# Performance work log

Hardware: AMD Instinct MI355X
Metric: run time of the kernel (lower is better)

## Reference

```python
import jax, jax.numpy as jnp
import numpy as np

N_NODES = 50000
N_EDGES = 800000
F_IN = 128
HID = 256
K = 5
N_GRAPHS = 64


def setup_inputs() -> dict:
    key = jax.random.key(0)
    ks = jax.random.split(key, 16)
    x = jax.random.normal(ks[0], (N_NODES, F_IN), dtype=jnp.float32)
    edge_index = jax.random.randint(ks[1], (2, N_EDGES), 0, N_NODES, dtype=jnp.int32)
    edge_weight = jax.random.uniform(ks[2], (N_EDGES,), dtype=jnp.float32)
    batch = jnp.sort(jax.random.randint(ks[3], (N_NODES,), 0, N_GRAPHS, dtype=jnp.int32))
    s = 0.05
    W1 = jax.random.normal(ks[4], (K, F_IN, HID), dtype=jnp.float32) * s
    b1 = jnp.zeros((HID,), dtype=jnp.float32)
    W2 = jax.random.normal(ks[5], (K, HID, HID), dtype=jnp.float32) * s
    b2 = jnp.zeros((HID,), dtype=jnp.float32)
    W3 = jax.random.normal(ks[6], (K, HID, HID), dtype=jnp.float32) * s
    b3 = jnp.zeros((HID,), dtype=jnp.float32)
    lw1 = jax.random.normal(ks[7], (HID, HID), dtype=jnp.float32) * s
    lb1 = jnp.zeros((HID,), dtype=jnp.float32)
    lw2 = jax.random.normal(ks[8], (HID, 1), dtype=jnp.float32) * s
    lb2 = jnp.zeros((1,), dtype=jnp.float32)
    return dict(x=x, edge_index=edge_index, edge_weight=edge_weight, batch=batch,
                W1=W1, b1=b1, W2=W2, b2=b2, W3=W3, b3=b3,
                lw1=lw1, lb1=lb1, lw2=lw2, lb2=lb2)


def _lap_weights(edge_index, edge_weight, num_nodes):
    # PyG ChebConv with normalization='sym', lambda_max=2.0:
    # L_hat = 2*L/lambda_max - I = -D^{-1/2} A D^{-1/2} on the off-diagonal,
    # zero diagonal. Degree via scatter on edge_index[0].
    src, dst = edge_index[0], edge_index[1]
    deg = jax.ops.segment_sum(edge_weight, src, num_segments=num_nodes)
    dis = jnp.where(deg > 0, jax.lax.rsqrt(jnp.maximum(deg, 1e-30)), 0.0)
    return -(dis[src] * edge_weight * dis[dst])


def _cheb_conv(x, src, dst, lap_w, W, b):
    # propagate: gather from src, weight, scatter-add to dst
    n = x.shape[0]
    prop = lambda z: jax.ops.segment_sum(lap_w[:, None] * z[src], dst, num_segments=n)
    Tx0 = x
    out = Tx0 @ W[0]
    Tx1 = prop(x)
    out = out + Tx1 @ W[1]
    for k in range(2, W.shape[0]):
        Tx2 = 2.0 * prop(Tx1) - Tx0
        out = out + Tx2 @ W[k]
        Tx0, Tx1 = Tx1, Tx2
    return out + b


def reference(x, edge_index, edge_weight, batch, W1, b1, W2, b2, W3, b3, lw1, lb1, lw2, lb2):
    src, dst = edge_index[0], edge_index[1]
    lap_w = _lap_weights(edge_index, edge_weight, x.shape[0])
    h = jax.nn.relu(_cheb_conv(x, src, dst, lap_w, W1, b1))
    h = _cheb_conv(h, src, dst, lap_w, W2, b2)
    h = jax.nn.relu(_cheb_conv(h, src, dst, lap_w, W3, b3))
    # global mean pool over graphs in the batch
    sums = jax.ops.segment_sum(h, batch, num_segments=N_GRAPHS)
    cnts = jax.ops.segment_sum(jnp.ones((h.shape[0],), h.dtype), batch, num_segments=N_GRAPHS)
    g = sums / jnp.maximum(cnts, 1.0)[:, None]
    g = jax.nn.relu(g)  # dropout is identity in eval mode
    g = g @ lw1 + lb1
    g = g @ lw2 + lb2
    return jax.nn.sigmoid(g)
```

## Files before the change

### kernel.cpp

```cpp
#include <hip/hip_runtime.h>
#include <math.h>

typedef unsigned int uint;
typedef unsigned short ushort;
typedef __bf16 bf16x8 __attribute__((ext_vector_type(8)));
typedef float f32x4 __attribute__((ext_vector_type(4)));
typedef __attribute__((address_space(1))) const void gvoid;
typedef __attribute__((address_space(3))) void svoid;

__device__ __forceinline__ float b2f(ushort u) {
  uint v = ((uint)u) << 16;
  return __uint_as_float(v);
}
__device__ __forceinline__ ushort f2b(float f) {
  uint u = __float_as_uint(f);
  u += 0x7FFFu + ((u >> 16) & 1u);
  return (ushort)(u >> 16);
}
__device__ __forceinline__ uint pack2(float a, float b) {
  return (uint)f2b(a) | ((uint)f2b(b) << 16);
}


__global__ void edge_kernel(const int* __restrict__ src, const int* __restrict__ dst,
                            const float* __restrict__ w, float* __restrict__ deg,
                            int* __restrict__ cnt, int ne) {
  int e = blockIdx.x * blockDim.x + threadIdx.x;
  if (e < ne) {
    atomicAdd(&deg[src[e]], w[e]);
    atomicAdd(&cnt[dst[e]], 1);
  }
}

__global__ __launch_bounds__(256) void node_kernel(float* __restrict__ deg,
                                                   const int* __restrict__ cnt,
                                                   int* __restrict__ rowstart,
                                                   int* __restrict__ cursor,
                                                   int* __restrict__ total,
                                                   const int* __restrict__ batch,
                                                   int nb, int ng, int* __restrict__ bnd) {
  __shared__ int ls[256];
  __shared__ int base;
  int tid = threadIdx.x;
  int i = blockIdx.x * 256 + tid;
  int c = (i < nb) ? cnt[i] : 0;
  ls[tid] = c;
  __syncthreads();
  for (int off = 1; off < 256; off <<= 1) {
    int v = (tid >= off) ? ls[tid - off] : 0;
    __syncthreads();
    ls[tid] += v;
    __syncthreads();
  }
  if (tid == 255) base = atomicAdd(total, ls[255]);
  __syncthreads();
  if (i < nb) {
    int pos = base + ls[tid] - c;
    rowstart[i] = pos;
    cursor[i] = pos;
    float d = deg[i];
    deg[i] = d > 0.f ? rsqrtf(fmaxf(d, 1e-30f)) : 0.f;
  }
  if (blockIdx.x == 0 && tid <= ng) {
    int lo = 0, hi = nb;
    while (lo < hi) {
      int mid = (lo + hi) >> 1;
      if (batch[mid] < tid) lo = mid + 1; else hi = mid;
    }
    bnd[tid] = lo;
  }
}

__global__ void scatter_kernel(const int* __restrict__ src, const int* __restrict__ dst,
                               const float* __restrict__ w, const float* __restrict__ dis,
                               int* __restrict__ cursor, int2* __restrict__ cv, int ne) {
  int e = blockIdx.x * blockDim.x + threadIdx.x;
  if (e < ne) {
    int d = dst[e], s = src[e];
    int pos = atomicAdd(&cursor[d], 1);
    float v = -(dis[s] * w[e] * dis[d]);
    cv[pos] = make_int2(s, __float_as_int(v));
  }
}


__global__ void xcvt_kernel(const float* __restrict__ x, uint* __restrict__ o, int total) {
  int i = blockIdx.x * blockDim.x + threadIdx.x;
  if (i < total) {
    float2 v = *(const float2*)(x + (size_t)i * 2);
    o[i] = pack2(v.x, v.y);
  }
}

__global__ void wprep_kernel(const float* __restrict__ W, ushort* __restrict__ WT,
                             int shift, int Ktot, int total) {
  int id = blockIdx.x * blockDim.x + threadIdx.x;
  if (id >= total) return;
  int n = id / Ktot;
  int k = id - n * Ktot;
  int fin = k & ((1 << shift) - 1);
  int ord = k >> shift;
  WT[id] = f2b(W[(size_t)(ord << shift) * 256 + (size_t)fin * 256 + n]);
}

__global__ void wprep2_kernel(const float* __restrict__ W2, ushort* __restrict__ WT2,
                              const float* __restrict__ W3, ushort* __restrict__ WT3,
                              int tot) {
  int id = blockIdx.x * blockDim.x + threadIdx.x;
  if (id >= 2 * tot) return;
  const float* W = (id < tot) ? W2 : W3;
  ushort* WT = (id < tot) ? WT2 : WT3;
  int t = (id < tot) ? id : id - tot;
  int n = t / 1280;
  int k = t - n * 1280;
  int fin = k & 255;
  int ord = k >> 8;
  WT[t] = f2b(W[(size_t)(ord << 8) * 256 + (size_t)fin * 256 + n]);
}


template <int WIDE>
__global__ __launch_bounds__(256) void spmm_wave(const int* __restrict__ rowstart,
                                                 const int* __restrict__ rowcnt,
                                                 const int2* __restrict__ cv,
                                                 const uint* __restrict__ X,
                                                 uint* __restrict__ out,
                                                 const uint* __restrict__ sub,
                                                 float alpha, int nb) {
  int row = blockIdx.x * 4 + (threadIdx.x >> 6);
  if (row >= nb) return;
  int lane = threadIdx.x & 63;
  int e0 = __builtin_amdgcn_readfirstlane(rowstart[row]);
  int cnt = __builtin_amdgcn_readfirstlane(rowcnt[row]);
  int e1 = e0 + cnt;
  float a0 = 0.f, a1 = 0.f, a2 = 0.f, a3 = 0.f;
  int e = e0;
  if (WIDE) {
    const uint2* Xr = (const uint2*)X;
    for (; e + 2 <= e1; e += 2) {
      int2 p0 = cv[e], p1 = cv[e + 1];
      int c0 = __builtin_amdgcn_readfirstlane(p0.x);
      float v0 = __uint_as_float(__builtin_amdgcn_readfirstlane((uint)p0.y));
      int c1 = __builtin_amdgcn_readfirstlane(p1.x);
      float v1 = __uint_as_float(__builtin_amdgcn_readfirstlane((uint)p1.y));
      uint2 g0 = Xr[(size_t)c0 * 64 + lane];
      uint2 g1 = Xr[(size_t)c1 * 64 + lane];
      a0 = fmaf(v0, b2f((ushort)(g0.x & 0xFFFF)), a0);
      a1 = fmaf(v0, b2f((ushort)(g0.x >> 16)), a1);
      a2 = fmaf(v0, b2f((ushort)(g0.y & 0xFFFF)), a2);
      a3 = fmaf(v0, b2f((ushort)(g0.y >> 16)), a3);
      a0 = fmaf(v1, b2f((ushort)(g1.x & 0xFFFF)), a0);
      a1 = fmaf(v1, b2f((ushort)(g1.x >> 16)), a1);
      a2 = fmaf(v1, b2f((ushort)(g1.y & 0xFFFF)), a2);
      a3 = fmaf(v1, b2f((ushort)(g1.y >> 16)), a3);
    }
    if (e < e1) {
      int2 p0 = cv[e];
      int c0 = __builtin_amdgcn_readfirstlane(p0.x);
      float v0 = __uint_as_float(__builtin_amdgcn_readfirstlane((uint)p0.y));
      uint2 g0 = Xr[(size_t)c0 * 64 + lane];
      a0 = fmaf(v0, b2f((ushort)(g0.x & 0xFFFF)), a0);
      a1 = fmaf(v0, b2f((ushort)(g0.x >> 16)), a1);
      a2 = fmaf(v0, b2f((ushort)(g0.y & 0xFFFF)), a2);
      a3 = fmaf(v0, b2f((ushort)(g0.y >> 16)), a3);
    }
    float r0 = alpha * a0, r1 = alpha * a1, r2 = alpha * a2, r3 = alpha * a3;
    if (sub) {
      uint2 s = ((const uint2*)sub)[(size_t)row * 64 + lane];
      r0 -= b2f((ushort)(s.x & 0xFFFF));
      r1 -= b2f((ushort)(s.x >> 16));
      r2 -= b2f((ushort)(s.y & 0xFFFF));
      r3 -= b2f((ushort)(s.y >> 16));
    }
    ((uint2*)out)[(size_t)row * 64 + lane] = make_uint2(pack2(r0, r1), pack2(r2, r3));
  } else {
    for (; e + 2 <= e1; e += 2) {
      int2 p0 = cv[e], p1 = cv[e + 1];
      int c0 = __builtin_amdgcn_readfirstlane(p0.x);
      float v0 = __uint_as_float(__builtin_amdgcn_readfirstlane((uint)p0.y));
      int c1 = __builtin_amdgcn_readfirstlane(p1.x);
      float v1 = __uint_as_float(__builtin_amdgcn_readfirstlane((uint)p1.y));
      uint g0 = X[(size_t)c0 * 64 + lane];
      uint g1 = X[(size_t)c1 * 64 + lane];
      a0 = fmaf(v0, b2f((ushort)(g0 & 0xFFFF)), a0);
      a1 = fmaf(v0, b2f((ushort)(g0 >> 16)), a1);
      a0 = fmaf(v1, b2f((ushort)(g1 & 0xFFFF)), a0);
      a1 = fmaf(v1, b2f((ushort)(g1 >> 16)), a1);
    }
    if (e < e1) {
      int2 p0 = cv[e];
      int c0 = __builtin_amdgcn_readfirstlane(p0.x);
      float v0 = __uint_as_float(__builtin_amdgcn_readfirstlane((uint)p0.y));
      uint g0 = X[(size_t)c0 * 64 + lane];
      a0 = fmaf(v0, b2f((ushort)(g0 & 0xFFFF)), a0);
      a1 = fmaf(v0, b2f((ushort)(g0 >> 16)), a1);
    }
    float r0 = alpha * a0, r1 = alpha * a1;
    if (sub) {
      uint s = sub[(size_t)row * 64 + lane];
      r0 -= b2f((ushort)(s & 0xFFFF));
      r1 -= b2f((ushort)(s >> 16));
    }
    out[(size_t)row * 64 + lane] = pack2(r0, r1);
  }
}


struct APtrs { const ushort* p[5]; };

template <int RELU, int SHIFT>
__global__ __launch_bounds__(256, 2) void gemm_mfma(APtrs ap, const ushort* __restrict__ WT,
                                                    const float* __restrict__ bias,
                                                    ushort* __restrict__ C, int M, int Ktot) {
  constexpr int LDA = 1 << SHIFT;
  __shared__ __align__(16) char lAb[16384];
  __shared__ __align__(16) char lBb[16384];
  int tid = threadIdx.x;
  int lane = tid & 63, w = tid >> 6;
  int wr = w >> 1, wc = w & 1;
  int row0 = blockIdx.x * 128, col0 = blockIdx.y * 128;

  f32x4 acc[4][4];
#pragma unroll
  for (int i = 0; i < 4; ++i)
#pragma unroll
    for (int n = 0; n < 4; ++n) acc[i][n] = {0.f, 0.f, 0.f, 0.f};

  for (int k0 = 0; k0 < Ktot; k0 += 64) {
    const ushort* Ab = ap.p[k0 >> SHIFT];
    int ka = k0 & (LDA - 1);
    __syncthreads();
#pragma unroll
    for (int c = 0; c < 4; ++c) {
      int base = c * 4096 + w * 1024;
      int off = base + lane * 16;
      int row = off >> 7, within = off & 127;
      int lw = within ^ ((row & 7) << 4);
      int grow = row0 + row; if (grow >= M) grow = M - 1;
      const ushort* g = Ab + (size_t)grow * LDA + ka + (lw >> 1);
      __builtin_amdgcn_global_load_lds((gvoid*)g, (svoid*)(lAb + base), 16, 0, 0);
    }
#pragma unroll
    for (int c = 0; c < 4; ++c) {
      int base = c * 4096 + w * 1024;
      int off = base + lane * 16;
      int n = off >> 7, within = off & 127;
      int lw = within ^ ((n & 7) << 4);
      const ushort* g = WT + (size_t)(col0 + n) * Ktot + k0 + (lw >> 1);
      __builtin_amdgcn_global_load_lds((gvoid*)g, (svoid*)(lBb + base), 16, 0, 0);
    }
    asm volatile("s_waitcnt vmcnt(0)" ::: "memory");
    __syncthreads();
#pragma unroll
    for (int s = 0; s < 2; ++s) {
      int kb = (s << 6) + ((lane >> 4) << 4);
      bf16x8 af[4], bfr[4];
#pragma unroll
      for (int i = 0; i < 4; ++i) {
        int mrow = (wr << 6) + (i << 4) + (lane & 15);
        af[i] = *(const bf16x8*)(lAb + (mrow << 7) + (kb ^ ((mrow & 7) << 4)));
      }
#pragma unroll
      for (int n = 0; n < 4; ++n) {
        int ncol = (wc << 6) + (n << 4) + (lane & 15);
        bfr[n] = *(const bf16x8*)(lBb + (ncol << 7) + (kb ^ ((ncol & 7) << 4)));
      }
#pragma unroll
      for (int i = 0; i < 4; ++i)
#pragma unroll
        for (int n = 0; n < 4; ++n)
          acc[i][n] = __builtin_amdgcn_mfma_f32_16x16x32_bf16(af[i], bfr[n], acc[i][n], 0, 0, 0);
    }
  }
  int cb = col0 + (wc << 6) + (lane & 15);
  float bv[4];
#pragma unroll
  for (int n = 0; n < 4; ++n) bv[n] = bias[cb + (n << 4)];
#pragma unroll
  for (int i = 0; i < 4; ++i) {
    int rbase = row0 + (wr << 6) + (i << 4) + ((lane >> 4) << 2);
#pragma unroll
    for (int r = 0; r < 4; ++r) {
      int row = rbase + r;
      if (row < M) {
#pragma unroll
        for (int n = 0; n < 4; ++n) {
          float v = acc[i][n][r] + bv[n];
          if (RELU) v = fmaxf(v, 0.f);
          C[(size_t)row * 256 + cb + (n << 4)] = f2b(v);
        }
      }
    }
  }
}


__global__ __launch_bounds__(256) void head_kernel(const uint* __restrict__ h,
                                                   const int* __restrict__ bnd,
                                                   const float* __restrict__ lw1,
                                                   const float* __restrict__ lb1,
                                                   const float* __restrict__ lw2,
                                                   const float* __restrict__ lb2,
                                                   float* __restrict__ out) {
  int g = blockIdx.x;
  int j = threadIdx.x;
  __shared__ float gs[256];
  __shared__ float red[256];
  int s = bnd[g], e = bnd[g + 1];
  int ui = j >> 1, half = j & 1;
  float acc = 0.f;
  int i = s;
  for (; i + 4 <= e; i += 4) {
    uint p0 = h[(size_t)(i + 0) * 128 + ui];
    uint p1 = h[(size_t)(i + 1) * 128 + ui];
    uint p2 = h[(size_t)(i + 2) * 128 + ui];
    uint p3 = h[(size_t)(i + 3) * 128 + ui];
    acc += b2f((ushort)(half ? (p0 >> 16) : (p0 & 0xFFFF)));
    acc += b2f((ushort)(half ? (p1 >> 16) : (p1 & 0xFFFF)));
    acc += b2f((ushort)(half ? (p2 >> 16) : (p2 & 0xFFFF)));
    acc += b2f((ushort)(half ? (p3 >> 16) : (p3 & 0xFFFF)));
  }
  for (; i < e; ++i) {
    uint p = h[(size_t)i * 128 + ui];
    acc += b2f((ushort)(half ? (p >> 16) : (p & 0xFFFF)));
  }
  float c = fmaxf((float)(e - s), 1.f);
  gs[j] = fmaxf(acc / c, 0.f);
  __syncthreads();
  float t = lb1[j];
  for (int k = 0; k < 256; ++k) t = fmaf(gs[k], lw1[k * 256 + j], t);
  red[j] = t * lw2[j];
  __syncthreads();
  for (int off = 128; off > 0; off >>= 1) {
    if (j < off) red[j] += red[j + off];
    __syncthreads();
  }
  if (j == 0) out[g] = 1.f / (1.f + expf(-(red[0] + lb2[0])));
}


extern "C" void kernel_launch(void* const* d_in, const int* in_sizes, int n_in,
                              void* d_out, int out_size, void* d_ws, size_t ws_size,
                              hipStream_t stream) {
  const float* x    = (const float*)d_in[0];
  const int*   ei   = (const int*)d_in[1];
  const float* ew   = (const float*)d_in[2];
  const int*   batch= (const int*)d_in[3];
  const float* W1 = (const float*)d_in[4];
  const float* b1 = (const float*)d_in[5];
  const float* W2 = (const float*)d_in[6];
  const float* b2 = (const float*)d_in[7];
  const float* W3 = (const float*)d_in[8];
  const float* b3 = (const float*)d_in[9];
  const float* lw1 = (const float*)d_in[10];
  const float* lb1 = (const float*)d_in[11];
  const float* lw2 = (const float*)d_in[12];
  const float* lb2 = (const float*)d_in[13];
  float* out = (float*)d_out;

  const int NE  = in_sizes[2];
  const int NB  = in_sizes[3];
  const int FIN = in_sizes[0] / NB;
  const int NG  = out_size;
  const int* src = ei;
  const int* dst = ei + NE;

  char* p = (char*)d_ws;
  auto alloc = [&](size_t bytes) {
    char* q = p;
    p += (bytes + 255) & ~(size_t)255;
    return q;
  };
  char* zb = (char*)alloc((size_t)(2 * NB + 1) * 4);
  float* deg  = (float*)zb;
  int*   cnt  = (int*)(zb + (size_t)NB * 4);
  int*   total= (int*)(zb + (size_t)2 * NB * 4);
  int*   rowstart = (int*)alloc((size_t)NB * 4);
  int*   cursor   = (int*)alloc((size_t)NB * 4);
  int2*  cv       = (int2*)alloc((size_t)NE * 8);
  int*   bnd      = (int*)alloc((size_t)(NG + 1) * 4);
  uint*  X0  = (uint*)alloc((size_t)NB * (FIN / 2) * 4);
  uint*  T1  = (uint*)alloc((size_t)NB * 128 * 4);
  uint*  T2  = (uint*)alloc((size_t)NB * 128 * 4);
  uint*  T3  = (uint*)alloc((size_t)NB * 128 * 4);
  uint*  T4  = (uint*)alloc((size_t)NB * 128 * 4);
  uint*  HA  = (uint*)alloc((size_t)NB * 128 * 4);
  uint*  HB  = (uint*)alloc((size_t)NB * 128 * 4);
  ushort* WT1 = (ushort*)alloc((size_t)256 * 5 * FIN * 2);
  ushort* WT2 = (ushort*)alloc((size_t)256 * 5 * 256 * 2);
  ushort* WT3 = (ushort*)alloc((size_t)256 * 5 * 256 * 2);

  hipMemsetAsync(zb, 0, (size_t)(2 * NB + 1) * 4, stream);

  int eb = (NE + 255) / 256;
  int nbb = (NB + 255) / 256;
  edge_kernel<<<eb, 256, 0, stream>>>(src, dst, ew, deg, cnt, NE);
  node_kernel<<<nbb, 256, 0, stream>>>(deg, cnt, rowstart, cursor, total, batch, NB, NG, bnd);
  scatter_kernel<<<eb, 256, 0, stream>>>(src, dst, ew, deg, cursor, cv, NE);

  int xcnt = NB * (FIN / 2);
  xcvt_kernel<<<(xcnt + 255) / 256, 256, 0, stream>>>(x, X0, xcnt);
  {
    int kt1 = 5 * FIN, tot1 = 256 * kt1;
    wprep_kernel<<<(tot1 + 255) / 256, 256, 0, stream>>>(W1, WT1, 7, kt1, tot1);
    int tot2 = 256 * 1280;
    wprep2_kernel<<<(2 * tot2 + 255) / 256, 256, 0, stream>>>(W2, WT2, W3, WT3, tot2);
  }

  int sgrid = (NB + 3) / 4;
  dim3 ggrid((NB + 127) / 128, 2);

  spmm_wave<0><<<sgrid, 256, 0, stream>>>(rowstart, cnt, cv, X0, T1, nullptr, 1.f, NB);
  spmm_wave<0><<<sgrid, 256, 0, stream>>>(rowstart, cnt, cv, T1, T2, X0, 2.f, NB);
  spmm_wave<0><<<sgrid, 256, 0, stream>>>(rowstart, cnt, cv, T2, T3, T1, 2.f, NB);
  spmm_wave<0><<<sgrid, 256, 0, stream>>>(rowstart, cnt, cv, T3, T4, T2, 2.f, NB);
  {
    APtrs ap = {{(const ushort*)X0, (const ushort*)T1, (const ushort*)T2,
                 (const ushort*)T3, (const ushort*)T4}};
    gemm_mfma<1, 7><<<ggrid, 256, 0, stream>>>(ap, WT1, b1, (ushort*)HA, NB, 5 * FIN);
  }
  spmm_wave<1><<<sgrid, 256, 0, stream>>>(rowstart, cnt, cv, HA, T1, nullptr, 1.f, NB);
  spmm_wave<1><<<sgrid, 256, 0, stream>>>(rowstart, cnt, cv, T1, T2, HA, 2.f, NB);
  spmm_wave<1><<<sgrid, 256, 0, stream>>>(rowstart, cnt, cv, T2, T3, T1, 2.f, NB);
  spmm_wave<1><<<sgrid, 256, 0, stream>>>(rowstart, cnt, cv, T3, T4, T2, 2.f, NB);
  {
    APtrs ap = {{(const ushort*)HA, (const ushort*)T1, (const ushort*)T2,
                 (const ushort*)T3, (const ushort*)T4}};
    gemm_mfma<0, 8><<<ggrid, 256, 0, stream>>>(ap, WT2, b2, (ushort*)HB, NB, 5 * 256);
  }
  spmm_wave<1><<<sgrid, 256, 0, stream>>>(rowstart, cnt, cv, HB, T1, nullptr, 1.f, NB);
  spmm_wave<1><<<sgrid, 256, 0, stream>>>(rowstart, cnt, cv, T1, T2, HB, 2.f, NB);
  spmm_wave<1><<<sgrid, 256, 0, stream>>>(rowstart, cnt, cv, T2, T3, T1, 2.f, NB);
  spmm_wave<1><<<sgrid, 256, 0, stream>>>(rowstart, cnt, cv, T3, T4, T2, 2.f, NB);
  {
    APtrs ap = {{(const ushort*)HB, (const ushort*)T1, (const ushort*)T2,
                 (const ushort*)T3, (const ushort*)T4}};
    gemm_mfma<1, 8><<<ggrid, 256, 0, stream>>>(ap, WT3, b3, (ushort*)HA, NB, 5 * 256);
  }

  head_kernel<<<NG, 256, 0, stream>>>(HA, bnd, lw1, lb1, lw2, lb2, out);
}
```

Before: 1.054 ms.

## Slice feature matrices into 32-column panels for cache-resident SpMM gathers

```diff
diff --git a/kernel.cpp b/kernel.cpp
--- a/kernel.cpp
+++ b/kernel.cpp
@@ -20,6 +20,7 @@
 __device__ __forceinline__ uint pack2(float a, float b) {
   return (uint)f2b(a) | ((uint)f2b(b) << 16);
 }
+
 
 
 __global__ void edge_kernel(const int* __restrict__ src, const int* __restrict__ dst,
@@ -84,12 +85,12 @@
 }
 
 
-__global__ void xcvt_kernel(const float* __restrict__ x, uint* __restrict__ o, int total) {
-  int i = blockIdx.x * blockDim.x + threadIdx.x;
-  if (i < total) {
-    float2 v = *(const float2*)(x + (size_t)i * 2);
-    o[i] = pack2(v.x, v.y);
-  }
+__global__ void xcvt_kernel(const float* __restrict__ x, uint* __restrict__ o, int nb) {
+  int id = blockIdx.x * blockDim.x + threadIdx.x;
+  if (id >= nb * 64) return;
+  int i = id >> 6, u = id & 63;
+  float2 v = *(const float2*)(x + (size_t)i * 128 + u * 2);
+  o[((size_t)(u >> 4) * nb + i) * 16 + (u & 15)] = pack2(v.x, v.y);
 }
 
 __global__ void wprep_kernel(const float* __restrict__ W, ushort* __restrict__ WT,
@@ -119,89 +120,57 @@
 }
 
 
-template <int WIDE>
-__global__ __launch_bounds__(256) void spmm_wave(const int* __restrict__ rowstart,
-                                                 const int* __restrict__ rowcnt,
-                                                 const int2* __restrict__ cv,
-                                                 const uint* __restrict__ X,
-                                                 uint* __restrict__ out,
-                                                 const uint* __restrict__ sub,
-                                                 float alpha, int nb) {
-  int row = blockIdx.x * 4 + (threadIdx.x >> 6);
+template <int LOG2NS>
+__global__ __launch_bounds__(256) void spmm_slice(const int* __restrict__ rowstart,
+                                                  const int* __restrict__ rowcnt,
+                                                  const int2* __restrict__ cv,
+                                                  const uint* __restrict__ X,
+                                                  uint* __restrict__ out,
+                                                  const uint* __restrict__ sub,
+                                                  float alpha, int nb) {
+  constexpr int NS = 1 << LOG2NS;
+  int s = blockIdx.x & (NS - 1);
+  int row = (blockIdx.x >> LOG2NS) * 4 + (threadIdx.x >> 6);
   if (row >= nb) return;
-  int lane = threadIdx.x & 63;
+  int l = threadIdx.x & 63;
+  int g = l >> 4, u = l & 15;
   int e0 = __builtin_amdgcn_readfirstlane(rowstart[row]);
   int cnt = __builtin_amdgcn_readfirstlane(rowcnt[row]);
   int e1 = e0 + cnt;
-  float a0 = 0.f, a1 = 0.f, a2 = 0.f, a3 = 0.f;
-  int e = e0;
-  if (WIDE) {
-    const uint2* Xr = (const uint2*)X;
-    for (; e + 2 <= e1; e += 2) {
-      int2 p0 = cv[e], p1 = cv[e + 1];
-      int c0 = __builtin_amdgcn_readfirstlane(p0.x);
-      float v0 = __uint_as_float(__builtin_amdgcn_readfirstlane((uint)p0.y));
-      int c1 = __builtin_amdgcn_readfirstlane(p1.x);
-      float v1 = __uint_as_float(__builtin_amdgcn_readfirstlane((uint)p1.y));
-      uint2 g0 = Xr[(size_t)c0 * 64 + lane];
-      uint2 g1 = Xr[(size_t)c1 * 64 + lane];
-      a0 = fmaf(v0, b2f((ushort)(g0.x & 0xFFFF)), a0);
-      a1 = fmaf(v0, b2f((ushort)(g0.x >> 16)), a1);
-      a2 = fmaf(v0, b2f((ushort)(g0.y & 0xFFFF)), a2);
-      a3 = fmaf(v0, b2f((ushort)(g0.y >> 16)), a3);
-      a0 = fmaf(v1, b2f((ushort)(g1.x & 0xFFFF)), a0);
-      a1 = fmaf(v1, b2f((ushort)(g1.x >> 16)), a1);
-      a2 = fmaf(v1, b2f((ushort)(g1.y & 0xFFFF)), a2);
-      a3 = fmaf(v1, b2f((ushort)(g1.y >> 16)), a3);
-    }
-    if (e < e1) {
-      int2 p0 = cv[e];
-      int c0 = __builtin_amdgcn_readfirstlane(p0.x);
-      float v0 = __uint_as_float(__builtin_amdgcn_readfirstlane((uint)p0.y));
-      uint2 g0 = Xr[(size_t)c0 * 64 + lane];
-      a0 = fmaf(v0, b2f((ushort)(g0.x & 0xFFFF)), a0);
-      a1 = fmaf(v0, b2f((ushort)(g0.x >> 16)), a1);
-      a2 = fmaf(v0, b2f((ushort)(g0.y & 0xFFFF)), a2);
-      a3 = fmaf(v0, b2f((ushort)(g0.y >> 16)), a3);
-    }
-    float r0 = alpha * a0, r1 = alpha * a1, r2 = alpha * a2, r3 = alpha * a3;
+  const uint* Xs = X + (size_t)s * nb * 16;
+  float a0 = 0.f, a1 = 0.f;
+  int e = e0 + g;
+  for (; e + 4 < e1; e += 8) {
+    int2 p0 = cv[e];
+    int2 p1 = cv[e + 4];
+    uint x0 = Xs[(size_t)p0.x * 16 + u];
+    uint x1 = Xs[(size_t)p1.x * 16 + u];
+    float v0 = __int_as_float(p0.y), v1 = __int_as_float(p1.y);
+    a0 = fmaf(v0, b2f((ushort)(x0 & 0xFFFF)), a0);
+    a1 = fmaf(v0, b2f((ushort)(x0 >> 16)), a1);
+    a0 = fmaf(v1, b2f((ushort)(x1 & 0xFFFF)), a0);
+    a1 = fmaf(v1, b2f((ushort)(x1 >> 16)), a1);
+  }
+  if (e < e1) {
+    int2 p0 = cv[e];
+    uint x0 = Xs[(size_t)p0.x * 16 + u];
+    float v0 = __int_as_float(p0.y);
+    a0 = fmaf(v0, b2f((ushort)(x0 & 0xFFFF)), a0);
+    a1 = fmaf(v0, b2f((ushort)(x0 >> 16)), a1);
+  }
+  a0 += __shfl_xor(a0, 16, 64);
+  a0 += __shfl_xor(a0, 32, 64);
+  a1 += __shfl_xor(a1, 16, 64);
+  a1 += __shfl_xor(a1, 32, 64);
+  if (g == 0) {
+    float r0 = alpha * a0, r1 = alpha * a1;
+    size_t oi = ((size_t)s * nb + row) * 16 + u;
     if (sub) {
-      uint2 s = ((const uint2*)sub)[(size_t)row * 64 + lane];
-      r0 -= b2f((ushort)(s.x & 0xFFFF));
-      r1 -= b2f((ushort)(s.x >> 16));
-      r2 -= b2f((ushort)(s.y & 0xFFFF));
-      r3 -= b2f((ushort)(s.y >> 16));
-    }
-    ((uint2*)out)[(size_t)row * 64 + lane] = make_uint2(pack2(r0, r1), pack2(r2, r3));
-  } else {
-    for (; e + 2 <= e1; e += 2) {
-      int2 p0 = cv[e], p1 = cv[e + 1];
-      int c0 = __builtin_amdgcn_readfirstlane(p0.x);
-      float v0 = __uint_as_float(__builtin_amdgcn_readfirstlane((uint)p0.y));
-      int c1 = __builtin_amdgcn_readfirstlane(p1.x);
-      float v1 = __uint_as_float(__builtin_amdgcn_readfirstlane((uint)p1.y));
-      uint g0 = X[(size_t)c0 * 64 + lane];
-      uint g1 = X[(size_t)c1 * 64 + lane];
-      a0 = fmaf(v0, b2f((ushort)(g0 & 0xFFFF)), a0);
-      a1 = fmaf(v0, b2f((ushort)(g0 >> 16)), a1);
-      a0 = fmaf(v1, b2f((ushort)(g1 & 0xFFFF)), a0);
-      a1 = fmaf(v1, b2f((ushort)(g1 >> 16)), a1);
-    }
-    if (e < e1) {
-      int2 p0 = cv[e];
-      int c0 = __builtin_amdgcn_readfirstlane(p0.x);
-      float v0 = __uint_as_float(__builtin_amdgcn_readfirstlane((uint)p0.y));
-      uint g0 = X[(size_t)c0 * 64 + lane];
-      a0 = fmaf(v0, b2f((ushort)(g0 & 0xFFFF)), a0);
-      a1 = fmaf(v0, b2f((ushort)(g0 >> 16)), a1);
-    }
-    float r0 = alpha * a0, r1 = alpha * a1;
-    if (sub) {
-      uint s = sub[(size_t)row * 64 + lane];
-      r0 -= b2f((ushort)(s & 0xFFFF));
-      r1 -= b2f((ushort)(s >> 16));
-    }
-    out[(size_t)row * 64 + lane] = pack2(r0, r1);
+      uint sv = sub[oi];
+      r0 -= b2f((ushort)(sv & 0xFFFF));
+      r1 -= b2f((ushort)(sv >> 16));
+    }
+    out[oi] = pack2(r0, r1);
   }
 }
 
@@ -227,7 +196,7 @@
     for (int n = 0; n < 4; ++n) acc[i][n] = {0.f, 0.f, 0.f, 0.f};
 
   for (int k0 = 0; k0 < Ktot; k0 += 64) {
-    const ushort* Ab = ap.p[k0 >> SHIFT];
+    const char* Ab = (const char*)ap.p[k0 >> SHIFT];
     int ka = k0 & (LDA - 1);
     __syncthreads();
 #pragma unroll
@@ -237,7 +206,8 @@
       int row = off >> 7, within = off & 127;
       int lw = within ^ ((row & 7) << 4);
       int grow = row0 + row; if (grow >= M) grow = M - 1;
-      const ushort* g = Ab + (size_t)grow * LDA + ka + (lw >> 1);
+      int rb = (ka << 1) + lw;
+      const char* g = Ab + ((size_t)(rb >> 6) * M + grow) * 64 + (rb & 63);
       __builtin_amdgcn_global_load_lds((gvoid*)g, (svoid*)(lAb + base), 16, 0, 0);
     }
 #pragma unroll
@@ -287,7 +257,8 @@
         for (int n = 0; n < 4; ++n) {
           float v = acc[i][n][r] + bv[n];
           if (RELU) v = fmaxf(v, 0.f);
-          C[(size_t)row * 256 + cb + (n << 4)] = f2b(v);
+          int c = cb + (n << 4);
+          C[((size_t)(c >> 5) * M + row) * 32 + ((c >> 1) & 15) * 2 + (c & 1)] = f2b(v);
         }
       }
     }
@@ -301,27 +272,28 @@
                                                    const float* __restrict__ lb1,
                                                    const float* __restrict__ lw2,
                                                    const float* __restrict__ lb2,
-                                                   float* __restrict__ out) {
+                                                   float* __restrict__ out, int nb) {
   int g = blockIdx.x;
   int j = threadIdx.x;
   __shared__ float gs[256];
   __shared__ float red[256];
   int s = bnd[g], e = bnd[g + 1];
   int ui = j >> 1, half = j & 1;
+  const uint* hs = h + (size_t)(ui >> 4) * nb * 16 + (ui & 15);
   float acc = 0.f;
   int i = s;
   for (; i + 4 <= e; i += 4) {
-    uint p0 = h[(size_t)(i + 0) * 128 + ui];
-    uint p1 = h[(size_t)(i + 1) * 128 + ui];
-    uint p2 = h[(size_t)(i + 2) * 128 + ui];
-    uint p3 = h[(size_t)(i + 3) * 128 + ui];
+    uint p0 = hs[(size_t)(i + 0) * 16];
+    uint p1 = hs[(size_t)(i + 1) * 16];
+    uint p2 = hs[(size_t)(i + 2) * 16];
+    uint p3 = hs[(size_t)(i + 3) * 16];
     acc += b2f((ushort)(half ? (p0 >> 16) : (p0 & 0xFFFF)));
     acc += b2f((ushort)(half ? (p1 >> 16) : (p1 & 0xFFFF)));
     acc += b2f((ushort)(half ? (p2 >> 16) : (p2 & 0xFFFF)));
     acc += b2f((ushort)(half ? (p3 >> 16) : (p3 & 0xFFFF)));
   }
   for (; i < e; ++i) {
-    uint p = h[(size_t)i * 128 + ui];
+    uint p = hs[(size_t)i * 16];
     acc += b2f((ushort)(half ? (p >> 16) : (p & 0xFFFF)));
   }
   float c = fmaxf((float)(e - s), 1.f);
@@ -398,8 +370,7 @@
   node_kernel<<<nbb, 256, 0, stream>>>(deg, cnt, rowstart, cursor, total, batch, NB, NG, bnd);
   scatter_kernel<<<eb, 256, 0, stream>>>(src, dst, ew, deg, cursor, cv, NE);
 
-  int xcnt = NB * (FIN / 2);
-  xcvt_kernel<<<(xcnt + 255) / 256, 256, 0, stream>>>(x, X0, xcnt);
+  xcvt_kernel<<<(NB * 64 + 255) / 256, 256, 0, stream>>>(x, X0, NB);
   {
     int kt1 = 5 * FIN, tot1 = 256 * kt1;
     wprep_kernel<<<(tot1 + 255) / 256, 256, 0, stream>>>(W1, WT1, 7, kt1, tot1);
@@ -407,36 +378,36 @@
     wprep2_kernel<<<(2 * tot2 + 255) / 256, 256, 0, stream>>>(W2, WT2, W3, WT3, tot2);
   }
 
-  int sgrid = (NB + 3) / 4;
+  int rb4 = (NB + 3) / 4;
   dim3 ggrid((NB + 127) / 128, 2);
 
-  spmm_wave<0><<<sgrid, 256, 0, stream>>>(rowstart, cnt, cv, X0, T1, nullptr, 1.f, NB);
-  spmm_wave<0><<<sgrid, 256, 0, stream>>>(rowstart, cnt, cv, T1, T2, X0, 2.f, NB);
-  spmm_wave<0><<<sgrid, 256, 0, stream>>>(rowstart, cnt, cv, T2, T3, T1, 2.f, NB);
-  spmm_wave<0><<<sgrid, 256, 0, stream>>>(rowstart, cnt, cv, T3, T4, T2, 2.f, NB);
+  spmm_slice<2><<<4 * rb4, 256, 0, stream>>>(rowstart, cnt, cv, X0, T1, nullptr, 1.f, NB);
+  spmm_slice<2><<<4 * rb4, 256, 0, stream>>>(rowstart, cnt, cv, T1, T2, X0, 2.f, NB);
+  spmm_slice<2><<<4 * rb4, 256, 0, stream>>>(rowstart, cnt, cv, T2, T3, T1, 2.f, NB);
+  spmm_slice<2><<<4 * rb4, 256, 0, stream>>>(rowstart, cnt, cv, T3, T4, T2, 2.f, NB);
   {
     APtrs ap = {{(const ushort*)X0, (const ushort*)T1, (const ushort*)T2,
                  (const ushort*)T3, (const ushort*)T4}};
     gemm_mfma<1, 7><<<ggrid, 256, 0, stream>>>(ap, WT1, b1, (ushort*)HA, NB, 5 * FIN);
   }
-  spmm_wave<1><<<sgrid, 256, 0, stream>>>(rowstart, cnt, cv, HA, T1, nullptr, 1.f, NB);
-  spmm_wave<1><<<sgrid, 256, 0, stream>>>(rowstart, cnt, cv, T1, T2, HA, 2.f, NB);
-  spmm_wave<1><<<sgrid, 256, 0, stream>>>(rowstart, cnt, cv, T2, T3, T1, 2.f, NB);
-  spmm_wave<1><<<sgrid, 256, 0, stream>>>(rowstart, cnt, cv, T3, T4, T2, 2.f, NB);
+  spmm_slice<3><<<8 * rb4, 256, 0, stream>>>(rowstart, cnt, cv, HA, T1, nullptr, 1.f, NB);
+  spmm_slice<3><<<8 * rb4, 256, 0, stream>>>(rowstart, cnt, cv, T1, T2, HA, 2.f, NB);
+  spmm_slice<3><<<8 * rb4, 256, 0, stream>>>(rowstart, cnt, cv, T2, T3, T1, 2.f, NB);
+  spmm_slice<3><<<8 * rb4, 256, 0, stream>>>(rowstart, cnt, cv, T3, T4, T2, 2.f, NB);
   {
     APtrs ap = {{(const ushort*)HA, (const ushort*)T1, (const ushort*)T2,
                  (const ushort*)T3, (const ushort*)T4}};
     gemm_mfma<0, 8><<<ggrid, 256, 0, stream>>>(ap, WT2, b2, (ushort*)HB, NB, 5 * 256);
   }
-  spmm_wave<1><<<sgrid, 256, 0, stream>>>(rowstart, cnt, cv, HB, T1, nullptr, 1.f, NB);
-  spmm_wave<1><<<sgrid, 256, 0, stream>>>(rowstart, cnt, cv, T1, T2, HB, 2.f, NB);
-  spmm_wave<1><<<sgrid, 256, 0, stream>>>(rowstart, cnt, cv, T2, T3, T1, 2.f, NB);
-  spmm_wave<1><<<sgrid, 256, 0, stream>>>(rowstart, cnt, cv, T3, T4, T2, 2.f, NB);
+  spmm_slice<3><<<8 * rb4, 256, 0, stream>>>(rowstart, cnt, cv, HB, T1, nullptr, 1.f, NB);
+  spmm_slice<3><<<8 * rb4, 256, 0, stream>>>(rowstart, cnt, cv, T1, T2, HB, 2.f, NB);
+  spmm_slice<3><<<8 * rb4, 256, 0, stream>>>(rowstart, cnt, cv, T2, T3, T1, 2.f, NB);
+  spmm_slice<3><<<8 * rb4, 256, 0, stream>>>(rowstart, cnt, cv, T3, T4, T2, 2.f, NB);
   {
     APtrs ap = {{(const ushort*)HB, (const ushort*)T1, (const ushort*)T2,
                  (const ushort*)T3, (const ushort*)T4}};
     gemm_mfma<1, 8><<<ggrid, 256, 0, stream>>>(ap, WT3, b3, (ushort*)HA, NB, 5 * 256);
   }
 
-  head_kernel<<<NG, 256, 0, stream>>>(HA, bnd, lw1, lb1, lw2, lb2, out);
-}
+  head_kernel<<<NG, 256, 0, stream>>>(HA, bnd, lw1, lb1, lw2, lb2, out, NB);
+}
```

Result: slower. 1.909 ms (+81.2%).
